# Kernel optimization log

Measured on AMD Instinct MI355X. Metric: run time of the kernel, lower is better.

The kernel has to match this reference:

```python
import jax, jax.numpy as jnp
import numpy as np

B, T, H, N = 1, 256, 32, 128
HN = H * N
KVH = 8
KV_DIM = KVH * N
KV_REPEAT = HN // KV_DIM
ROPE_THETA = 10000.0
EPS = 1e-6
NTK_ALPHA = 10.0
YARN_MAX = 4096.0
LORA_W, LORA_A, LORA_V, LORA_G = 64, 64, 32, 128
LAYER_ID = 1


def t5_rmsnorm(x, w):
    xf = x.astype(jnp.float32)
    var = jnp.mean(xf * xf, axis=-1, keepdims=True)
    return (w * (xf * jax.lax.rsqrt(var + EPS))).astype(x.dtype)


def rotate_half(x):
    h = x.shape[-1] // 2
    return jnp.concatenate([-x[..., h:], x[..., :h]], axis=-1)


def rope_cache(cache_pos, seq_len, rotary_dim):
    # YaRN-style mix of short/long inv_freq, per compute_rope_cache_range
    half = rotary_dim // 2
    fs = jnp.arange(half, dtype=jnp.float32)
    inv_short = 1.0 / ROPE_THETA ** (fs / half)
    inv_long = 1.0 / (ROPE_THETA * NTK_ALPHA ** (fs / half))
    pos = cache_pos.astype(jnp.float32) + jnp.arange(seq_len, dtype=jnp.float32)[None, :]  # [B,T]
    mix = jnp.clip(pos / YARN_MAX, 0.0, 1.0)[..., None]
    freqs = (1.0 - mix) * (pos[..., None] * inv_short) + mix * (pos[..., None] * inv_long)
    emb = jnp.concatenate([freqs, freqs], axis=-1)  # [B,T,rotary_dim]
    return jnp.cos(emb), jnp.sin(emb)


def _forward(x_in, v_first, state, cache_position, w0, w1, w2, a0, a1, a2, v0, v1, v2, g1, g2,
             r_k, R_, K_, V_, O_, R_bias, K_bias, V_bias, ln_r, ln_k, ln1, ln2):
    x = t5_rmsnorm(x_in, ln1)  # [B,T,HN]
    # float path of fpx_matmul: x @ W.T (+ bias), i.e. the dequantized math
    r = x @ R_.T + R_bias
    k = x @ K_.T + K_bias
    v = x @ V_.T + V_bias
    r = t5_rmsnorm(r.reshape(B, T, H, N), ln_r)      # [B,T,H,N]
    k = t5_rmsnorm(k.reshape(B, T, KVH, N), ln_k)    # [B,T,KVH,N]
    cos, sin = rope_cache(cache_position, T, N)      # [B,T,N]
    cos_, sin_ = cos[:, :, None, :], sin[:, :, None, :]
    r = r * cos_ + rotate_half(r) * sin_
    k = k * cos_ + rotate_half(k) * sin_
    # decay lora: w = -softplus(-(tanh(x@w1)@w2 + w0)) - 0.5
    w = jnp.tanh(x @ w1) @ w2 + w0
    w = -jax.nn.softplus(-w) - 0.5
    # GQA repeat_kv: each kv head repeated KV_REPEAT times contiguously
    v = v.reshape(B, T, KVH, N)
    k = jnp.repeat(k, KV_REPEAT, axis=2).reshape(B, T, HN)
    v = jnp.repeat(v, KV_REPEAT, axis=2).reshape(B, T, HN)
    a = jax.nn.sigmoid((x @ a1) @ a2 + a0)
    g = jax.nn.sigmoid(x @ g1) @ g2
    k4 = k.reshape(B, T, H, N)
    kk = (k4 / jnp.maximum(jnp.linalg.norm(k4, axis=-1, keepdims=True), 1e-12)).reshape(B, T, HN)
    k = k * (1.0 - w + a)
    aa = -kk
    bb = kk * a
    if LAYER_ID == 0:
        v_first = v
    else:
        gate = jax.nn.sigmoid((x @ v1) @ v2 + v0)
        v = v + (v_first - v) * gate
    w = -jnp.exp(w.astype(jnp.float32))  # log-decay for the recurrence

    def to_tm(t):  # [B,T,HN] or [B,T,H,N] -> time-major [T,B,H,N]
        return jnp.moveaxis(t.reshape(B, T, H, N), 1, 0)

    rt, wt, kt, vt, at, bt = map(to_tm, (r, w, k, v, aa, bb))

    def step(S, inp):
        # RWKV-7: S = S*diag(exp(w)) + S @ (a b^T) + v k^T ; out = S @ r
        r_t, w_t, k_t, v_t, a_t, b_t = inp
        sa = jnp.einsum('bhij,bhj->bhi', S, a_t)
        S = S * jnp.exp(w_t)[:, :, None, :] + sa[..., None] * b_t[:, :, None, :] + v_t[..., None] * k_t[:, :, None, :]
        return S, jnp.einsum('bhij,bhj->bhi', S, r_t)

    S_final, outs = jax.lax.scan(step, state.astype(jnp.float32), (rt, wt, kt, vt, at, bt))
    xx = jnp.moveaxis(outs, 0, 1).reshape(B, T, HN) * (float(N) ** -0.5)
    bonus = jnp.sum(r.reshape(B, T, H, N) * k.reshape(B, T, H, N) * r_k, axis=-1, keepdims=True) * v.reshape(B, T, H, N)
    xx = xx.astype(r.dtype) + bonus.reshape(B, T, HN)
    x_res = x_in + (xx * g) @ O_.T
    out = t5_rmsnorm(x_res, ln2)
    return out, x[:, -1], S_final, v_first, x_res


def setup_inputs() -> dict:
    key = jax.random.key(0)
    ks = iter(jax.random.split(key, 32))
    rn = lambda *s: jax.random.normal(next(ks), s, dtype=jnp.float32)
    wt = lambda *s: rn(*s) * 0.02
    return dict(
        x_in=rn(B, T, HN),
        v_first=rn(B, T, HN),
        state=jnp.zeros((B, H, N, N), jnp.float32),
        cache_position=jnp.zeros((B, 1), jnp.int32),
        w0=wt(HN), w1=wt(HN, LORA_W), w2=wt(LORA_W, HN),
        a0=wt(HN), a1=wt(HN, LORA_A), a2=wt(LORA_A, HN),
        v0=wt(HN), v1=wt(HN, LORA_V), v2=wt(LORA_V, HN),
        g1=wt(HN, LORA_G), g2=wt(LORA_G, HN),
        r_k=wt(H, N),
        R_=wt(HN, HN), K_=wt(KV_DIM, HN), V_=wt(KV_DIM, HN), O_=wt(HN, HN),
        R_bias=wt(HN), K_bias=wt(KV_DIM), V_bias=wt(KV_DIM),
        ln_r=jnp.ones((N,), jnp.float32), ln_k=jnp.ones((N,), jnp.float32),
        ln1=jnp.ones((HN,), jnp.float32), ln2=jnp.ones((HN,), jnp.float32),
    )


def reference(x_in, v_first, state, cache_position, w0, w1, w2, a0, a1, a2, v0, v1, v2, g1, g2,
              r_k, R_, K_, V_, O_, R_bias, K_bias, V_bias, ln_r, ln_k, ln1, ln2):
    return _forward(x_in, v_first, state, cache_position, w0, w1, w2, a0, a1, a2, v0, v1, v2,
                    g1, g2, r_k, R_, K_, V_, O_, R_bias, K_bias, V_bias, ln_r, ln_k, ln1, ln2)
```

## Files before the change

kernel.cpp:

```cpp
#include <hip/hip_runtime.h>
#include <cstdint>
#include <cstddef>

#define T_ 256
#define HN_ 4096
#define H_ 32
#define N_ 128
#define SR_ 6464

typedef __attribute__((ext_vector_type(8))) short short8;
typedef __attribute__((ext_vector_type(4))) float f32x4;

__device__ __forceinline__ short f2bf(float f) {
    uint32_t u = __builtin_bit_cast(uint32_t, f);
    u = (u + 0x7fffu + ((u >> 16) & 1u)) >> 16;
    return (short)u;
}
__device__ __forceinline__ short f2bfc(float f) {
    return (short)((__builtin_bit_cast(uint32_t, f) + 0x8000u) >> 16);
}
__device__ __forceinline__ short8 cvt8r(float4 lo, float4 hi) {
    short8 v;
    v[0] = f2bfc(lo.x); v[1] = f2bfc(lo.y); v[2] = f2bfc(lo.z); v[3] = f2bfc(lo.w);
    v[4] = f2bfc(hi.x); v[5] = f2bfc(hi.y); v[6] = f2bfc(hi.z); v[7] = f2bfc(hi.w);
    return v;
}
__device__ __forceinline__ f32x4 mfma16(short8 a, short8 b, f32x4 c) {
    return __builtin_amdgcn_mfma_f32_16x16x32_bf16(a, b, c, 0, 0, 0);
}
__device__ __forceinline__ float sigm(float x) { return 1.f / (1.f + expf(-x)); }
__device__ __forceinline__ float splus(float x) { return (x > 20.f) ? x : log1pf(expf(x)); }

__device__ __forceinline__ float bf1(ushort u) {
    return __builtin_bit_cast(float, (uint32_t)u << 16);
}
__device__ __forceinline__ void gload_lds16(const void* g, void* l) {
    __builtin_amdgcn_global_load_lds(
        (const __attribute__((address_space(1))) void*)g,
        (__attribute__((address_space(3))) void*)l, 16, 0, 0);
}

template <int CTRL>
__device__ __forceinline__ float dpp_add(float v) {
    int p = __builtin_amdgcn_mov_dpp(__builtin_bit_cast(int, v), CTRL, 0xF, 0xF, true);
    return v + __builtin_bit_cast(float, p);
}
__device__ __forceinline__ float reduce64(float v) {
    v = dpp_add<0xB1>(v);
    v = dpp_add<0x4E>(v);
    v = dpp_add<0x124>(v);
    v = dpp_add<0x128>(v);
    v = dpp_add<0x142>(v);
    v = dpp_add<0x143>(v);
    int r = __builtin_amdgcn_readlane(__builtin_bit_cast(int, v), 63);
    return __builtin_bit_cast(float, r);
}

__device__ __forceinline__ void gemm_core(
    const ushort* __restrict__ A, const float* __restrict__ Brow,
    int kbeg, ushort* LH, f32x4 acc[2][2]) {
    const int tid = threadIdx.x, wid = tid >> 6, l = tid & 63;
    const int ar = l & 15, ak = (l >> 4) * 8;
    const int mBase = wid * 32;

    const int brw = tid >> 4, bc8 = tid & 15;
    const float* bsrc = Brow + (size_t)brw * 4096 + kbeg + bc8 * 8;
    const int hoff = brw * 128 + ((bc8 ^ (brw & 7)) * 8);

    const ushort* pa0 = A + (size_t)(mBase + ar) * 4096 + kbeg + ak;
    const ushort* pa1 = pa0 + (size_t)16 * 4096;

    const int akc = ak >> 3;
    const int sx0 = ar & 7;
    const int rb0 = ar * 128, rb1 = (16 + ar) * 128;

    short8 Ae[8], Ao[8];
    float4 B0a, B0b, B1a, B1b;

#define LB0(s) { B0a = *(const float4*)(bsrc + (size_t)(s) * 128); \
                 B0b = *(const float4*)(bsrc + (size_t)(s) * 128 + 4); }
#define LB1(s) { B1a = *(const float4*)(bsrc + (size_t)(s) * 128); \
                 B1b = *(const float4*)(bsrc + (size_t)(s) * 128 + 4); }

#define LA(B_, s) { \
    B_[0] = *(const short8*)(pa0 + (size_t)(s) * 128);      \
    B_[1] = *(const short8*)(pa1 + (size_t)(s) * 128);      \
    B_[2] = *(const short8*)(pa0 + (size_t)(s) * 128 + 32); \
    B_[3] = *(const short8*)(pa1 + (size_t)(s) * 128 + 32); \
    B_[4] = *(const short8*)(pa0 + (size_t)(s) * 128 + 64); \
    B_[5] = *(const short8*)(pa1 + (size_t)(s) * 128 + 64); \
    B_[6] = *(const short8*)(pa0 + (size_t)(s) * 128 + 96); \
    B_[7] = *(const short8*)(pa1 + (size_t)(s) * 128 + 96); }

#define CKK(kk, B_, Hb_) { \
    const int sl = ((kk) * 4 + akc) ^ sx0; \
    short8 b0 = *(const short8*)((Hb_) + rb0 + sl * 8); \
    short8 b1 = *(const short8*)((Hb_) + rb1 + sl * 8); \
    acc[0][0] = mfma16(B_[2 * (kk)], b0, acc[0][0]); \
    acc[0][1] = mfma16(B_[2 * (kk)], b1, acc[0][1]); \
    acc[1][0] = mfma16(B_[2 * (kk) + 1], b0, acc[1][0]); \
    acc[1][1] = mfma16(B_[2 * (kk) + 1], b1, acc[1][1]); }

#define COMPUTE(Hb_, B_) { CKK(0, B_, Hb_) CKK(1, B_, Hb_) CKK(2, B_, Hb_) CKK(3, B_, Hb_) }

    LB0(0)
    LA(Ae, 0)
    LB1(1)

    for (int su = 0; su < 4; su++) {
        const int s0 = su * 2, s1 = su * 2 + 1;

        *(short8*)(LH + hoff) = cvt8r(B0a, B0b);
        LB0((s0 + 2 < 8) ? s0 + 2 : 7)
        LA(Ao, s0 + 1)
        asm volatile("s_waitcnt lgkmcnt(0)" ::: "memory");
        __builtin_amdgcn_s_barrier();
        __builtin_amdgcn_sched_barrier(0);
        COMPUTE(LH, Ae)

        *(short8*)(LH + 4096 + hoff) = cvt8r(B1a, B1b);
        LB1((s1 + 2 < 8) ? s1 + 2 : 7)
        LA(Ae, (s1 + 1 < 8) ? s1 + 1 : 7)
        asm volatile("s_waitcnt lgkmcnt(0)" ::: "memory");
        __builtin_amdgcn_s_barrier();
        __builtin_amdgcn_sched_barrier(0);
        COMPUTE(LH + 4096, Ao)
    }
#undef LB0
#undef LB1
#undef LA
#undef CKK
#undef COMPUTE
}

__global__ __launch_bounds__(256) void rmsnorm_k(const float* __restrict__ in,
                                                 const float* __restrict__ w,
                                                 float* __restrict__ outF,
                                                 ushort* __restrict__ outB,
                                                 float* __restrict__ lastrow) {
    int t = blockIdx.x, tid = threadIdx.x;
    const float4* in4 = (const float4*)(in + (size_t)t * HN_);
    const float4* w4 = (const float4*)w;
    float4 v[4]; float ss = 0.f;
#pragma unroll
    for (int q = 0; q < 4; q++) {
        v[q] = in4[q * 256 + tid];
        ss += v[q].x * v[q].x + v[q].y * v[q].y + v[q].z * v[q].z + v[q].w * v[q].w;
    }
#pragma unroll
    for (int o = 32; o; o >>= 1) ss += __shfl_down(ss, o);
    __shared__ float red[4];
    if ((tid & 63) == 0) red[tid >> 6] = ss;
    __syncthreads();
    float tot = red[0] + red[1] + red[2] + red[3];
    float sc = rsqrtf(tot * (1.f / HN_) + 1e-6f);
#pragma unroll
    for (int q = 0; q < 4; q++) {
        float4 wv = w4[q * 256 + tid];
        float4 r;
        r.x = wv.x * v[q].x * sc; r.y = wv.y * v[q].y * sc;
        r.z = wv.z * v[q].z * sc; r.w = wv.w * v[q].w * sc;
        int idx = q * 256 + tid;
        if (outF) ((float4*)(outF + (size_t)t * HN_))[idx] = r;
        if (outB) {
            ushort4 b;
            b.x = (ushort)f2bf(r.x); b.y = (ushort)f2bf(r.y);
            b.z = (ushort)f2bf(r.z); b.w = (ushort)f2bf(r.w);
            ((ushort4*)(outB + (size_t)t * HN_))[idx] = b;
        }
        if (lastrow && t == T_ - 1) ((float4*)lastrow)[idx] = r;
    }
}

__global__ __launch_bounds__(512, 2) void gemm_rkvt(
    const ushort* __restrict__ A,
    const float* __restrict__ Rw, const float* __restrict__ Kw,
    const float* __restrict__ Vw, const float* __restrict__ WT,
    float* __restrict__ COMB) {
    __shared__ __align__(16) ushort LH[8192];
    const int tid = threadIdx.x, wid = tid >> 6, l = tid & 63;
    const int mBase = wid * 32;
    const int nB = blockIdx.x * 32;
    const int kbeg = blockIdx.y * 1024;

    const float* Bp; int brow;
    if (nB < 4096)      { Bp = Rw; brow = nB; }
    else if (nB < 5120) { Bp = Kw; brow = nB - 4096; }
    else if (nB < 6144) { Bp = Vw; brow = nB - 5120; }
    else                { Bp = WT; brow = nB - 6144; }

    f32x4 acc[2][2];
#pragma unroll
    for (int i = 0; i < 2; i++)
#pragma unroll
        for (int j = 0; j < 2; j++) acc[i][j] = f32x4{0.f, 0.f, 0.f, 0.f};

    gemm_core(A, Bp + (size_t)brow * 4096, kbeg, LH, acc);

    const int rl = (l >> 4) * 4, cl = l & 15;
#pragma unroll
    for (int mf = 0; mf < 2; mf++)
#pragma unroll
        for (int nf = 0; nf < 2; nf++)
#pragma unroll
            for (int e = 0; e < 4; e++)
                unsafeAtomicAdd(&COMB[(size_t)(mBase + mf * 16 + rl + e) * SR_ + nB + nf * 16 + cl],
                                acc[mf][nf][e]);
}

__global__ __launch_bounds__(512, 2) void gemm_o(
    const ushort* __restrict__ A,
    const float* __restrict__ B,
    float* __restrict__ C) {
    __shared__ __align__(16) ushort LH[8192];
    const int tid = threadIdx.x, wid = tid >> 6, l = tid & 63;
    const int mBase = wid * 32;
    const int nB = blockIdx.x * 32;
    const int kbeg = blockIdx.y * 1024;

    f32x4 acc[2][2];
#pragma unroll
    for (int i = 0; i < 2; i++)
#pragma unroll
        for (int j = 0; j < 2; j++) acc[i][j] = f32x4{0.f, 0.f, 0.f, 0.f};

    gemm_core(A, B + (size_t)nB * 4096, kbeg, LH, acc);

    const int rl = (l >> 4) * 4, cl = l & 15;
#pragma unroll
    for (int mf = 0; mf < 2; mf++)
#pragma unroll
        for (int nf = 0; nf < 2; nf++)
#pragma unroll
            for (int e = 0; e < 4; e++)
                unsafeAtomicAdd(&C[(size_t)(mBase + mf * 16 + rl + e) * 4096 + nB + nf * 16 + cl],
                                acc[mf][nf][e]);
}

__global__ __launch_bounds__(512) void gemm_s2(
    const ushort* __restrict__ TCB,
    const float* __restrict__ w2, const float* __restrict__ a2,
    const float* __restrict__ v2, const float* __restrict__ g2,
    const float* __restrict__ w0, const float* __restrict__ a0,
    const float* __restrict__ v0,
    float* __restrict__ WPRE, float* __restrict__ APRE,
    float* __restrict__ VGPRE, float* __restrict__ GARR) {
    const int z = blockIdx.y;
    int Aoff, K; const float* B; const float* bias; float* out;
    if (z == 0)      { Aoff = 0;   K = 64;  B = w2; bias = w0;      out = WPRE; }
    else if (z == 1) { Aoff = 64;  K = 64;  B = a2; bias = a0;      out = APRE; }
    else if (z == 2) { Aoff = 128; K = 32;  B = v2; bias = v0;      out = VGPRE; }
    else             { Aoff = 160; K = 128; B = g2; bias = nullptr; out = GARR; }

    const int tid = threadIdx.x, wid = tid >> 6, l = tid & 63;
    const int ar = l & 15, ak = (l >> 4) * 8;
    const int mBase = wid * 32;
    const int nB = blockIdx.x * 32;

    f32x4 acc[2][2];
#pragma unroll
    for (int i = 0; i < 2; i++)
#pragma unroll
        for (int j = 0; j < 2; j++) acc[i][j] = f32x4{0.f, 0.f, 0.f, 0.f};

    for (int k0 = 0; k0 < K; k0 += 32) {
        const ushort* pA = TCB + (size_t)(mBase + ar) * 320 + Aoff + k0 + ak;
        short8 av0 = *(const short8*)pA;
        short8 av1 = *(const short8*)(pA + (size_t)16 * 320);
        short8 bv0, bv1;
#pragma unroll
        for (int e = 0; e < 8; e++) {
            bv0[e] = f2bfc(B[(size_t)(k0 + ak + e) * 4096 + nB + ar]);
            bv1[e] = f2bfc(B[(size_t)(k0 + ak + e) * 4096 + nB + 16 + ar]);
        }
        acc[0][0] = mfma16(av0, bv0, acc[0][0]);
        acc[0][1] = mfma16(av0, bv1, acc[0][1]);
        acc[1][0] = mfma16(av1, bv0, acc[1][0]);
        acc[1][1] = mfma16(av1, bv1, acc[1][1]);
    }
    const int rl = (l >> 4) * 4, cl = l & 15;
#pragma unroll
    for (int mf = 0; mf < 2; mf++)
#pragma unroll
        for (int nf = 0; nf < 2; nf++) {
            int col = nB + nf * 16 + cl;
            float bv = bias ? bias[col] : 0.f;
#pragma unroll
            for (int e = 0; e < 4; e++)
                out[(size_t)(mBase + mf * 16 + rl + e) * 4096 + col] = acc[mf][nf][e] + bv;
        }
}

__global__ __launch_bounds__(256) void wcat2_k(const float* __restrict__ w1p,
                                               const float* __restrict__ a1p,
                                               const float* __restrict__ v1p,
                                               const float* __restrict__ g1p,
                                               float* __restrict__ WT) {
    const int kb = blockIdx.x * 64, tile = blockIdx.y;
    const float* src; int ldw, jo, nb, W;
    if (tile == 0)      { src = w1p; ldw = 64;  jo = 0;  nb = 0;   W = 64; }
    else if (tile == 1) { src = a1p; ldw = 64;  jo = 0;  nb = 64;  W = 64; }
    else if (tile == 2) { src = v1p; ldw = 32;  jo = 0;  nb = 128; W = 32; }
    else if (tile == 3) { src = g1p; ldw = 128; jo = 0;  nb = 160; W = 64; }
    else                { src = g1p; ldw = 128; jo = 64; nb = 224; W = 64; }
    __shared__ float lds[64][65];
    const int ti = threadIdx.x & 63, wi = threadIdx.x >> 6;
    if (ti < W)
        for (int i = wi; i < 64; i += 4)
            lds[i][ti] = src[(size_t)(kb + i) * ldw + jo + ti];
    __syncthreads();
    for (int i2 = wi; i2 < W; i2 += 4)
        WT[(size_t)(nb + i2) * 4096 + kb + ti] = lds[ti][i2];
}

__global__ __launch_bounds__(256) void init_comb_k(const float* __restrict__ Rb,
                                                   const float* __restrict__ Kb,
                                                   const float* __restrict__ Vb,
                                                   float* __restrict__ COMB) {
    int t = blockIdx.x;
    for (int c = threadIdx.x; c < SR_; c += 256) {
        float b = (c < 4096) ? Rb[c] : (c < 5120) ? Kb[c - 4096]
                : (c < 6144) ? Vb[c - 5120] : 0.f;
        COMB[(size_t)t * SR_ + c] = b;
    }
}

__global__ __launch_bounds__(256) void act_k(const float* __restrict__ COMB,
                                             ushort* __restrict__ TCB) {
    int idx = blockIdx.x * 256 + threadIdx.x;
    if (idx >= 256 * 288) return;
    int t = idx / 288, c = idx % 288;
    float v = COMB[(size_t)t * SR_ + 6144 + c];
    if (c < 64) v = tanhf(v);
    else if (c >= 160) v = sigm(v);
    TCB[t * 320 + c] = (ushort)f2bf(v);
}

__global__ __launch_bounds__(256) void prep_k(
    const float* __restrict__ COMB, const float* __restrict__ wpre,
    const float* __restrict__ apre, const float* __restrict__ vgpre,
    const float* __restrict__ vfirst, const float* __restrict__ garr,
    const float* __restrict__ rkg, const int* __restrict__ cpos,
    const float* __restrict__ lnr, const float* __restrict__ lnk,
    ushort* __restrict__ SFB) {
    const int tp = blockIdx.x, hg = blockIdx.y;
    const int tid = threadIdx.x;
    const int w = tid >> 6, lane = tid & 63;
    const int t0 = tp * 2, t1 = t0 + 1;

    float e = (float)lane * (1.f / 64.f);
    float inv_s = exp2f(-13.287712379549449f * e);
    float inv_l = exp2f(-13.287712379549449f - 3.321928094887362f * e);
    float base = (float)cpos[0];
    float pos0 = base + (float)t0, pos1 = base + (float)t1;
    float mix0 = fminf(fmaxf(pos0 * (1.f / 4096.f), 0.f), 1.f);
    float mix1 = fminf(fmaxf(pos1 * (1.f / 4096.f), 0.f), 1.f);
    float fr0 = pos0 * ((1.f - mix0) * inv_s + mix0 * inv_l);
    float fr1 = pos1 * ((1.f - mix1) * inv_s + mix1 * inv_l);
    float cA = cosf(fr0), sA = sinf(fr0);
    float cB = cosf(fr1), sB = sinf(fr1);

    float lr0 = lnr[lane], lr1 = lnr[lane + 64];
    float lk0 = lnk[lane], lk1 = lnk[lane + 64];

    for (int hb = hg * 4; hb < hg * 4 + 4; hb++) {
        int h = hb * 4 + w;
        int kv = h >> 2;
        float rk0 = rkg[h * 128 + lane], rk1 = rkg[h * 128 + 64 + lane];

        auto STEPQ = [&](int t, float cc, float ss,
                         float& Rr0, float& Rr1, float& Kf0, float& Kf1,
                         float& Aa0, float& Aa1, float& Bb0, float& Bb1,
                         float& Dd0, float& Dd1, float& Vv0, float& Vv1,
                         float& Gg0, float& Gg1) {
            size_t tS = (size_t)t * SR_;
            float r0 = COMB[tS + h * 128 + lane];
            float r1 = COMB[tS + h * 128 + 64 + lane];
            float sm = reduce64(r0 * r0 + r1 * r1);
            float sc = rsqrtf(sm * (1.f / 128.f) + 1e-6f);
            float rn0 = lr0 * r0 * sc, rn1 = lr1 * r1 * sc;
            Rr0 = rn0 * cc - rn1 * ss; Rr1 = rn1 * cc + rn0 * ss;
            float k0 = COMB[tS + 4096 + kv * 128 + lane];
            float k1 = COMB[tS + 4096 + kv * 128 + 64 + lane];
            float ks = reduce64(k0 * k0 + k1 * k1);
            float ksc = rsqrtf(ks * (1.f / 128.f) + 1e-6f);
            float kn0 = lk0 * k0 * ksc, kn1 = lk1 * k1 * ksc;
            float kr0 = kn0 * cc - kn1 * ss, kr1 = kn1 * cc + kn0 * ss;
            float nr = reduce64(kr0 * kr0 + kr1 * kr1);
            float inv = 1.f / fmaxf(sqrtf(nr), 1e-12f);
            float kk0 = kr0 * inv, kk1 = kr1 * inv;
            int ch0 = h * 128 + lane, ch1 = ch0 + 64;
            size_t tb = (size_t)t * HN_;
            float wv0 = -splus(-wpre[tb + ch0]) - 0.5f;
            float wv1 = -splus(-wpre[tb + ch1]) - 0.5f;
            Dd0 = expf(-expf(wv0)); Dd1 = expf(-expf(wv1));
            float av0 = sigm(apre[tb + ch0]);
            float av1 = sigm(apre[tb + ch1]);
            float vg0 = sigm(vgpre[tb + ch0]);
            float vg1 = sigm(vgpre[tb + ch1]);
            float vr0 = COMB[tS + 5120 + kv * 128 + lane];
            float vr1 = COMB[tS + 5120 + kv * 128 + 64 + lane];
            Vv0 = vr0 + (vfirst[tb + ch0] - vr0) * vg0;
            Vv1 = vr1 + (vfirst[tb + ch1] - vr1) * vg1;
            Kf0 = kr0 * (1.f - wv0 + av0); Kf1 = kr1 * (1.f - wv1 + av1);
            Aa0 = -kk0; Aa1 = -kk1;
            Bb0 = kk0 * av0; Bb1 = kk1 * av1;
            Gg0 = garr[tb + ch0]; Gg1 = garr[tb + ch1];
        };

        float r00, r01, k00, k01, a00, a01, b00, b01, d00, d01, v00, v01, g00, g01;
        float r10, r11, k10, k11, a10, a11, b10, b11, d10, d11, v10, v11, g10, g11;
        STEPQ(t0, cA, sA, r00, r01, k00, k01, a00, a01, b00, b01, d00, d01, v00, v01, g00, g01);
        STEPQ(t1, cB, sB, r10, r11, k10, k11, a10, a11, b10, b11, d10, d11, v10, v11, g10, g11);

        float* rf = (float*)(SFB + ((size_t)h * 128 + tp) * 3072);
        rf[0    + lane] = a00;        rf[0    + 64 + lane] = a01;
        rf[128  + lane] = d00 * a10;  rf[128  + 64 + lane] = d01 * a11;
        rf[256  + lane] = d00 * r00;  rf[256  + 64 + lane] = d01 * r01;
        rf[384  + lane] = r10;        rf[384  + 64 + lane] = r11;
        rf[512  + lane] = d00 * d10;  rf[512  + 64 + lane] = d01 * d11;
        rf[640  + lane] = b00 * d10;  rf[640  + 64 + lane] = b01 * d11;
        rf[768  + lane] = k00 * d10;  rf[768  + 64 + lane] = k01 * d11;
        rf[896  + lane] = b10;        rf[896  + 64 + lane] = b11;
        rf[1024 + lane] = k10;        rf[1024 + 64 + lane] = k11;
        ushort* us = (ushort*)rf;
        us[2304 + lane] = (ushort)f2bf(v00); us[2304 + 64 + lane] = (ushort)f2bf(v01);
        us[2432 + lane] = (ushort)f2bf(v10); us[2432 + 64 + lane] = (ushort)f2bf(v11);
        us[2560 + lane] = (ushort)f2bf(g00); us[2560 + 64 + lane] = (ushort)f2bf(g01);
        us[2688 + lane] = (ushort)f2bf(g10); us[2688 + 64 + lane] = (ushort)f2bf(g11);

        float C1  = reduce64(b00 * a10 + b01 * a11);
        float C2  = reduce64(k00 * a10 + k01 * a11);
        float C3  = reduce64(b00 * r00 + b01 * r01);
        float C4  = reduce64(k00 * r00 + k01 * r01);
        float BD0 = reduce64(r00 * k00 * rk0 + r01 * k01 * rk1);
        float BD1 = reduce64(r10 * k10 * rk0 + r11 * k11 * rk1);
        if (lane == 0) {
            rf[1408] = C1; rf[1409] = C2; rf[1410] = C3;
            rf[1411] = C4; rf[1412] = BD0; rf[1413] = BD1;
        }
    }
}

#define SDP_ 5
#define SNBP_ 6
__global__ __launch_bounds__(256) void scan_k(
    const float* __restrict__ state_in,
    const ushort* __restrict__ SFB,
    ushort* __restrict__ yb, float* __restrict__ Sout,
    ushort* __restrict__ dummy) {
    const int h = blockIdx.x, sp = blockIdx.y;
    const int tid = threadIdx.x;
    const int wv = tid >> 6, ln = tid & 63;
    const int i = sp * 4 + wv;
    const int j0 = ln * 2;

    float S0, S1;
    {
        float2 s2 = *(const float2*)(state_in + ((size_t)h * 128 + i) * 128 + j0);
        S0 = s2.x; S1 = s2.y;
    }

    __shared__ __align__(16) ushort lds_s[SNBP_][3072];
    const ushort* hbase = SFB + (size_t)h * 128 * 3072;

    auto STAGE = [&](int buf, int tp) {
        if (wv < 3) {
            const ushort* src = hbase + (size_t)(tp & 127) * 3072 + wv * 1024 + ln * 8;
            gload_lds16(src,       &lds_s[buf][wv * 1024]);
            gload_lds16(src + 512, &lds_s[buf][wv * 1024 + 512]);
        }
    };

#pragma unroll
    for (int d = 0; d < SDP_; d++) STAGE(d, d);

    float pend_y0 = 0.f, pend_y1 = 0.f;
    float r1c0 = 0.f, r1c1 = 0.f, bd1c = 0.f, vi1c = 0.f, gi1c = 0.f;
    for (int Io = 0; Io < 132; Io += 6) {
#pragma unroll
        for (int u = 0; u < 6; u++) {
            const int I = Io + u;
            if (I >= 128) break;
            const int bc = u;
            const int bs = (u + SDP_) % 6;

            if (wv < 3) {
                if (I < SDP_) asm volatile("s_waitcnt vmcnt(8)" ::: "memory");
                else          asm volatile("s_waitcnt vmcnt(16)" ::: "memory");
            }
            __builtin_amdgcn_s_barrier();
            __builtin_amdgcn_sched_barrier(0);
            asm volatile("" ::: "memory");

            if (ln == 0) {
                ushort* p0 = (I >= 1) ? (yb + (size_t)(2 * I - 2) * HN_ + h * 128 + i)
                                      : (dummy + tid);
                *p0 = (ushort)f2bf(pend_y0);
                ushort* p1 = (I >= 2) ? (yb + (size_t)(2 * I - 3) * HN_ + h * 128 + i)
                                      : (dummy + 256 + tid);
                *p1 = (ushort)f2bf(pend_y1);
            }

            STAGE(bs, I + SDP_);

            const ushort* L = lds_s[bc];
            const float* Lf = (const float*)L;
            float2 A0 = *(const float2*)(Lf + 0    + j0);
            float2 WA = *(const float2*)(Lf + 128  + j0);
            float2 WR = *(const float2*)(Lf + 256  + j0);
            float2 R1 = *(const float2*)(Lf + 384  + j0);
            float2 W2 = *(const float2*)(Lf + 512  + j0);
            float2 BW = *(const float2*)(Lf + 640  + j0);
            float2 KW = *(const float2*)(Lf + 768  + j0);
            float2 B1 = *(const float2*)(Lf + 896  + j0);
            float2 K1 = *(const float2*)(Lf + 1024 + j0);
            float vi0 = bf1(L[2304 + i]);
            float vi1 = bf1(L[2432 + i]);
            float gi0 = bf1(L[2560 + i]);
            float gi1 = bf1(L[2688 + i]);
            const float* Sc = Lf + 1408;
            float c1 = Sc[0], c2 = Sc[1], c3 = Sc[2], c4 = Sc[3];
            float bd0 = Sc[4], bd1 = Sc[5];

            float up = fmaf(S0, A0.x, S1 * A0.y);
            float pp = fmaf(S0, WA.x, S1 * WA.y);
            float yp = fmaf(S0, WR.x, S1 * WR.y);
            float op = fmaf(S0, r1c0, S1 * r1c1);
            float u_   = reduce64(up);
            float p_   = reduce64(pp);
            float yb0  = reduce64(yp);
            float od1  = reduce64(op);

            pend_y1 = fmaf(od1, 0.08838834764831845f, bd1c * vi1c) * gi1c;

            float sa0 = u_;
            float sa1 = fmaf(sa0, c1, fmaf(vi0, c2, p_));
            float od0 = fmaf(sa0, c3, fmaf(vi0, c4, yb0));
            pend_y0 = fmaf(od0, 0.08838834764831845f, bd0 * vi0) * gi0;

            S0 = fmaf(sa0, BW.x, S0 * W2.x);
            S0 = fmaf(vi0, KW.x, S0);
            S0 = fmaf(sa1, B1.x, S0);
            S0 = fmaf(vi1, K1.x, S0);
            S1 = fmaf(sa0, BW.y, S1 * W2.y);
            S1 = fmaf(vi0, KW.y, S1);
            S1 = fmaf(sa1, B1.y, S1);
            S1 = fmaf(vi1, K1.y, S1);

            r1c0 = R1.x; r1c1 = R1.y;
            bd1c = bd1; vi1c = vi1; gi1c = gi1;
        }
    }

    {
        float op = fmaf(S0, r1c0, S1 * r1c1);
        float od1 = reduce64(op);
        float cp1 = fmaf(od1, 0.08838834764831845f, bd1c * vi1c) * gi1c;
        if (ln == 0) {
            yb[(size_t)255 * HN_ + h * 128 + i] = (ushort)f2bf(cp1);
            yb[(size_t)254 * HN_ + h * 128 + i] = (ushort)f2bf(pend_y0);
            yb[(size_t)253 * HN_ + h * 128 + i] = (ushort)f2bf(pend_y1);
        }
    }

    float* pS = Sout + ((size_t)h * 128 + i) * 128 + j0;
    *(float2*)pS = make_float2(S0, S1);
}

extern "C" void kernel_launch(void* const* d_in, const int* in_sizes, int n_in,
                              void* d_out, int out_size, void* d_ws, size_t ws_size,
                              hipStream_t stream) {
    const float* x_in   = (const float*)d_in[0];
    const float* vfirst = (const float*)d_in[1];
    const float* state  = (const float*)d_in[2];
    const int*   cpos   = (const int*)d_in[3];
    const float* w0 = (const float*)d_in[4];
    const float* w1 = (const float*)d_in[5];
    const float* w2 = (const float*)d_in[6];
    const float* a0 = (const float*)d_in[7];
    const float* a1 = (const float*)d_in[8];
    const float* a2 = (const float*)d_in[9];
    const float* v0 = (const float*)d_in[10];
    const float* v1 = (const float*)d_in[11];
    const float* v2 = (const float*)d_in[12];
    const float* g1 = (const float*)d_in[13];
    const float* g2 = (const float*)d_in[14];
    const float* r_k = (const float*)d_in[15];
    const float* R_ = (const float*)d_in[16];
    const float* K_ = (const float*)d_in[17];
    const float* V_ = (const float*)d_in[18];
    const float* O_ = (const float*)d_in[19];
    const float* Rb = (const float*)d_in[20];
    const float* Kb = (const float*)d_in[21];
    const float* Vb = (const float*)d_in[22];
    const float* ln_r = (const float*)d_in[23];
    const float* ln_k = (const float*)d_in[24];
    const float* ln1 = (const float*)d_in[25];
    const float* ln2 = (const float*)d_in[26];

    float* ws = (float*)d_ws;
    constexpr size_t OFF_XB   = 0;
    constexpr size_t OFF_COMB = 524288;
    constexpr size_t OFF_WT   = 2179072;
    constexpr size_t OFF_TCB  = 3489792;
    constexpr size_t OFF_WPRE = 3530752;
    constexpr size_t OFF_APRE = 4579328;
    constexpr size_t OFF_VGPRE= 5627904;
    constexpr size_t OFF_G    = 6676480;
    constexpr size_t OFF_SF   = 7757824;
    constexpr size_t OFF_DUM  = 14049280;
    constexpr size_t OFF_YB   = OFF_XB;

    ushort* XB  = (ushort*)(ws + OFF_XB);
    float* COMB = ws + OFF_COMB;
    float* WT   = ws + OFF_WT;
    ushort* TCB = (ushort*)(ws + OFF_TCB);
    float* WPRE = ws + OFF_WPRE;
    float* APRE = ws + OFF_APRE;
    float* VGPRE= ws + OFF_VGPRE;
    float* GARR = ws + OFF_G;
    ushort* SFB = (ushort*)(ws + OFF_SF);
    ushort* DUM = (ushort*)(ws + OFF_DUM);
    ushort* YB  = (ushort*)(ws + OFF_YB);

    float* out = (float*)d_out;
    float* out0  = out;
    float* xlast = out + 1048576;
    float* Sfin  = out + 1052672;
    float* vfout = out + 1576960;
    float* xres  = out + 2625536;

    hipMemcpyAsync(vfout, vfirst, (size_t)1048576 * 4, hipMemcpyDeviceToDevice, stream);
    hipMemcpyAsync(xres, x_in, (size_t)1048576 * 4, hipMemcpyDeviceToDevice, stream);

    rmsnorm_k<<<T_, 256, 0, stream>>>(x_in, ln1, nullptr, XB, xlast);

    wcat2_k<<<dim3(64, 5), 256, 0, stream>>>(w1, a1, v1, g1, WT);
    hipMemsetAsync(WT + (size_t)288 * 4096, 0, (size_t)32 * 4096 * 4, stream);
    init_comb_k<<<T_, 256, 0, stream>>>(Rb, Kb, Vb, COMB);

    gemm_rkvt<<<dim3(202, 4), 512, 0, stream>>>(XB, R_, K_, V_, WT, COMB);

    act_k<<<288, 256, 0, stream>>>(COMB, TCB);

    gemm_s2<<<dim3(128, 4), 512, 0, stream>>>(TCB, w2, a2, v2, g2, w0, a0, v0,
                                              WPRE, APRE, VGPRE, GARR);

    prep_k<<<dim3(128, 2), 256, 0, stream>>>(COMB, WPRE, APRE, VGPRE, vfirst, GARR,
                                             r_k, cpos, ln_r, ln_k, SFB);

    scan_k<<<dim3(32, 32), 256, 0, stream>>>(state, SFB, YB, Sfin, DUM);

    gemm_o<<<dim3(128, 4), 512, 0, stream>>>(YB, O_, xres);

    rmsnorm_k<<<T_, 256, 0, stream>>>(xres, ln2, out0, nullptr, nullptr);
}
```

Baseline: 282.9 us.

## Replace LDS-staged scan pipeline with direct register double-buffered global loads

New measurement: 347.6 us. 22.9% more time.

```diff
diff --git a/kernel.cpp b/kernel.cpp
--- a/kernel.cpp
+++ b/kernel.cpp
@@ -33,11 +33,6 @@
 
 __device__ __forceinline__ float bf1(ushort u) {
     return __builtin_bit_cast(float, (uint32_t)u << 16);
-}
-__device__ __forceinline__ void gload_lds16(const void* g, void* l) {
-    __builtin_amdgcn_global_load_lds(
-        (const __attribute__((address_space(1))) void*)g,
-        (__attribute__((address_space(3))) void*)l, 16, 0, 0);
 }
 
 template <int CTRL>
@@ -442,13 +437,15 @@
     }
 }
 
-#define SDP_ 5
-#define SNBP_ 6
+struct Rec {
+    float2 A0, WA, WR, R1, W2, BW, KW, B1, K1;
+    float vi0, vi1, gi0, gi1;
+    float2 c12, c34, bdp;
+};
 __global__ __launch_bounds__(256) void scan_k(
     const float* __restrict__ state_in,
     const ushort* __restrict__ SFB,
-    ushort* __restrict__ yb, float* __restrict__ Sout,
-    ushort* __restrict__ dummy) {
+    ushort* __restrict__ yb, float* __restrict__ Sout) {
     const int h = blockIdx.x, sp = blockIdx.y;
     const int tid = threadIdx.x;
     const int wv = tid >> 6, ln = tid & 63;
@@ -461,96 +458,75 @@
         S0 = s2.x; S1 = s2.y;
     }
 
-    __shared__ __align__(16) ushort lds_s[SNBP_][3072];
     const ushort* hbase = SFB + (size_t)h * 128 * 3072;
 
-    auto STAGE = [&](int buf, int tp) {
-        if (wv < 3) {
-            const ushort* src = hbase + (size_t)(tp & 127) * 3072 + wv * 1024 + ln * 8;
-            gload_lds16(src,       &lds_s[buf][wv * 1024]);
-            gload_lds16(src + 512, &lds_s[buf][wv * 1024 + 512]);
-        }
+    auto LOADR = [&](Rec& R, int tp) {
+        const float* Lf = (const float*)(hbase + (size_t)tp * 3072);
+        const ushort* Lu = (const ushort*)Lf;
+        R.A0 = *(const float2*)(Lf + 0    + j0);
+        R.WA = *(const float2*)(Lf + 128  + j0);
+        R.WR = *(const float2*)(Lf + 256  + j0);
+        R.R1 = *(const float2*)(Lf + 384  + j0);
+        R.W2 = *(const float2*)(Lf + 512  + j0);
+        R.BW = *(const float2*)(Lf + 640  + j0);
+        R.KW = *(const float2*)(Lf + 768  + j0);
+        R.B1 = *(const float2*)(Lf + 896  + j0);
+        R.K1 = *(const float2*)(Lf + 1024 + j0);
+        R.vi0 = bf1(Lu[2304 + i]);
+        R.vi1 = bf1(Lu[2432 + i]);
+        R.gi0 = bf1(Lu[2560 + i]);
+        R.gi1 = bf1(Lu[2688 + i]);
+        R.c12 = *(const float2*)(Lf + 1408);
+        R.c34 = *(const float2*)(Lf + 1410);
+        R.bdp = *(const float2*)(Lf + 1412);
     };
-
-#pragma unroll
-    for (int d = 0; d < SDP_; d++) STAGE(d, d);
 
     float pend_y0 = 0.f, pend_y1 = 0.f;
     float r1c0 = 0.f, r1c1 = 0.f, bd1c = 0.f, vi1c = 0.f, gi1c = 0.f;
-    for (int Io = 0; Io < 132; Io += 6) {
-#pragma unroll
-        for (int u = 0; u < 6; u++) {
-            const int I = Io + u;
-            if (I >= 128) break;
-            const int bc = u;
-            const int bs = (u + SDP_) % 6;
-
-            if (wv < 3) {
-                if (I < SDP_) asm volatile("s_waitcnt vmcnt(8)" ::: "memory");
-                else          asm volatile("s_waitcnt vmcnt(16)" ::: "memory");
-            }
-            __builtin_amdgcn_s_barrier();
-            __builtin_amdgcn_sched_barrier(0);
-            asm volatile("" ::: "memory");
-
-            if (ln == 0) {
-                ushort* p0 = (I >= 1) ? (yb + (size_t)(2 * I - 2) * HN_ + h * 128 + i)
-                                      : (dummy + tid);
-                *p0 = (ushort)f2bf(pend_y0);
-                ushort* p1 = (I >= 2) ? (yb + (size_t)(2 * I - 3) * HN_ + h * 128 + i)
-                                      : (dummy + 256 + tid);
-                *p1 = (ushort)f2bf(pend_y1);
-            }
-
-            STAGE(bs, I + SDP_);
-
-            const ushort* L = lds_s[bc];
-            const float* Lf = (const float*)L;
-            float2 A0 = *(const float2*)(Lf + 0    + j0);
-            float2 WA = *(const float2*)(Lf + 128  + j0);
-            float2 WR = *(const float2*)(Lf + 256  + j0);
-            float2 R1 = *(const float2*)(Lf + 384  + j0);
-            float2 W2 = *(const float2*)(Lf + 512  + j0);
-            float2 BW = *(const float2*)(Lf + 640  + j0);
-            float2 KW = *(const float2*)(Lf + 768  + j0);
-            float2 B1 = *(const float2*)(Lf + 896  + j0);
-            float2 K1 = *(const float2*)(Lf + 1024 + j0);
-            float vi0 = bf1(L[2304 + i]);
-            float vi1 = bf1(L[2432 + i]);
-            float gi0 = bf1(L[2560 + i]);
-            float gi1 = bf1(L[2688 + i]);
-            const float* Sc = Lf + 1408;
-            float c1 = Sc[0], c2 = Sc[1], c3 = Sc[2], c4 = Sc[3];
-            float bd0 = Sc[4], bd1 = Sc[5];
-
-            float up = fmaf(S0, A0.x, S1 * A0.y);
-            float pp = fmaf(S0, WA.x, S1 * WA.y);
-            float yp = fmaf(S0, WR.x, S1 * WR.y);
-            float op = fmaf(S0, r1c0, S1 * r1c1);
-            float u_   = reduce64(up);
-            float p_   = reduce64(pp);
-            float yb0  = reduce64(yp);
-            float od1  = reduce64(op);
-
-            pend_y1 = fmaf(od1, 0.08838834764831845f, bd1c * vi1c) * gi1c;
-
-            float sa0 = u_;
-            float sa1 = fmaf(sa0, c1, fmaf(vi0, c2, p_));
-            float od0 = fmaf(sa0, c3, fmaf(vi0, c4, yb0));
-            pend_y0 = fmaf(od0, 0.08838834764831845f, bd0 * vi0) * gi0;
-
-            S0 = fmaf(sa0, BW.x, S0 * W2.x);
-            S0 = fmaf(vi0, KW.x, S0);
-            S0 = fmaf(sa1, B1.x, S0);
-            S0 = fmaf(vi1, K1.x, S0);
-            S1 = fmaf(sa0, BW.y, S1 * W2.y);
-            S1 = fmaf(vi0, KW.y, S1);
-            S1 = fmaf(sa1, B1.y, S1);
-            S1 = fmaf(vi1, K1.y, S1);
-
-            r1c0 = R1.x; r1c1 = R1.y;
-            bd1c = bd1; vi1c = vi1; gi1c = gi1;
-        }
+
+    auto STEP = [&](const Rec& R, int I) {
+        if (ln == 0 && I >= 1)
+            yb[(size_t)(2 * I - 2) * HN_ + h * 128 + i] = (ushort)f2bf(pend_y0);
+        if (ln == 0 && I >= 2)
+            yb[(size_t)(2 * I - 3) * HN_ + h * 128 + i] = (ushort)f2bf(pend_y1);
+
+        float up = fmaf(S0, R.A0.x, S1 * R.A0.y);
+        float pp = fmaf(S0, R.WA.x, S1 * R.WA.y);
+        float yp = fmaf(S0, R.WR.x, S1 * R.WR.y);
+        float op = fmaf(S0, r1c0, S1 * r1c1);
+        float u_   = reduce64(up);
+        float p_   = reduce64(pp);
+        float yb0  = reduce64(yp);
+        float od1  = reduce64(op);
+
+        pend_y1 = fmaf(od1, 0.08838834764831845f, bd1c * vi1c) * gi1c;
+
+        float sa0 = u_;
+        float sa1 = fmaf(sa0, R.c12.x, fmaf(R.vi0, R.c12.y, p_));
+        float od0 = fmaf(sa0, R.c34.x, fmaf(R.vi0, R.c34.y, yb0));
+        pend_y0 = fmaf(od0, 0.08838834764831845f, R.bdp.x * R.vi0) * R.gi0;
+
+        S0 = fmaf(sa0, R.BW.x, S0 * R.W2.x);
+        S0 = fmaf(R.vi0, R.KW.x, S0);
+        S0 = fmaf(sa1, R.B1.x, S0);
+        S0 = fmaf(R.vi1, R.K1.x, S0);
+        S1 = fmaf(sa0, R.BW.y, S1 * R.W2.y);
+        S1 = fmaf(R.vi0, R.KW.y, S1);
+        S1 = fmaf(sa1, R.B1.y, S1);
+        S1 = fmaf(R.vi1, R.K1.y, S1);
+
+        r1c0 = R.R1.x; r1c1 = R.R1.y;
+        bd1c = R.bdp.y; vi1c = R.vi1; gi1c = R.gi1;
+    };
+
+    Rec RA, RB;
+    LOADR(RA, 0);
+    LOADR(RB, 1);
+    for (int I = 0; I < 128; I += 2) {
+        STEP(RA, I);
+        if (I + 2 < 128) LOADR(RA, I + 2);
+        STEP(RB, I + 1);
+        if (I + 3 < 128) LOADR(RB, I + 3);
     }
 
     {
@@ -609,7 +585,6 @@
     constexpr size_t OFF_VGPRE= 5627904;
     constexpr size_t OFF_G    = 6676480;
     constexpr size_t OFF_SF   = 7757824;
-    constexpr size_t OFF_DUM  = 14049280;
     constexpr size_t OFF_YB   = OFF_XB;
 
     ushort* XB  = (ushort*)(ws + OFF_XB);
@@ -621,7 +596,6 @@
     float* VGPRE= ws + OFF_VGPRE;
     float* GARR = ws + OFF_G;
     ushort* SFB = (ushort*)(ws + OFF_SF);
-    ushort* DUM = (ushort*)(ws + OFF_DUM);
     ushort* YB  = (ushort*)(ws + OFF_YB);
 
     float* out = (float*)d_out;
@@ -650,7 +624,7 @@
     prep_k<<<dim3(128, 2), 256, 0, stream>>>(COMB, WPRE, APRE, VGPRE, vfirst, GARR,
                                              r_k, cpos, ln_r, ln_k, SFB);
 
-    scan_k<<<dim3(32, 32), 256, 0, stream>>>(state, SFB, YB, Sfin, DUM);
+    scan_k<<<dim3(32, 32), 256, 0, stream>>>(state, SFB, YB, Sfin);
 
     gemm_o<<<dim3(128, 4), 512, 0, stream>>>(YB, O_, xres);
 
```
